# Performance work log

Hardware: AMD Instinct MI355X
Metric: run time of the kernel (lower is better)

Reference implementation:

```python
import jax, jax.numpy as jnp
import numpy as np

S = 128          # spatial grid size per axis
N = 100000       # active voxels
C_IN = 32
C_OUT = 32
FS = 3           # filter size per axis -> 27 offsets


def _build_rulebook():
    """Build submanifold-conv rulebook: for each active site and each of the
    27 filter offsets, the index of the active neighbor (or masked out)."""
    rng = np.random.default_rng(0)
    coords = rng.integers(0, S, size=(2 * N, 3))
    lin = coords[:, 0] * S * S + coords[:, 1] * S + coords[:, 2]
    lin = np.unique(lin)[:N]                      # sorted unique active sites
    xyz = np.stack([lin // (S * S), (lin // S) % S, lin % S], axis=1)  # [N,3]
    offs = np.stack(np.meshgrid(*([np.arange(FS) - FS // 2] * 3), indexing='ij'), -1).reshape(-1, 3)  # [27,3]
    nb = xyz[:, None, :] + offs[None, :, :]       # [N,27,3]
    inb = np.all((nb >= 0) & (nb < S), axis=-1)   # in-bounds
    nb_lin = nb[..., 0] * S * S + nb[..., 1] * S + nb[..., 2]
    pos = np.searchsorted(lin, nb_lin)
    pos_c = np.clip(pos, 0, N - 1)
    found = inb & (lin[pos_c] == nb_lin)
    nbr_idx = np.where(found, pos_c, 0).astype(np.int32)   # [N,27]
    return nbr_idx, found


def setup_inputs() -> dict:
    key = jax.random.key(0)
    k1, k2 = jax.random.split(key)
    nbr_idx, nbr_mask = _build_rulebook()
    K = FS ** 3
    std = (2.0 / C_IN / K) ** 0.5   # matches module init
    return {
        'features': jax.random.normal(k1, (N, C_IN), dtype=jnp.float32),
        'weight': std * jax.random.normal(k2, (K, C_IN, C_OUT), dtype=jnp.float32),
        'bias': jnp.zeros((C_OUT,), dtype=jnp.float32),
        'nbr_idx': jnp.asarray(nbr_idx),
        'nbr_mask': jnp.asarray(nbr_mask),
    }


def reference(features, weight, bias, nbr_idx, nbr_mask):
    # Submanifold sparse conv: gather active neighbors per filter offset,
    # multiply by per-offset [Cin,Cout] weight, accumulate at active sites.
    gathered = jnp.where(nbr_mask[:, :, None], features[nbr_idx], 0.0)  # [N,K,Cin]
    out = jnp.einsum('nki,kio->no', gathered, weight) + bias            # [N,Cout]
    return out
```

## Files before the change

kernel.cpp:

```cpp
#include <hip/hip_runtime.h>
#include <hip/hip_bf16.h>

#define NVOX 100000
#define CIN 32
#define COUT 32
#define KOFF 27
#define NTILE 6250
#define SENTE (NVOX << 6)

typedef __attribute__((ext_vector_type(8))) short short8;
typedef __attribute__((ext_vector_type(4))) float float4v;
typedef __attribute__((ext_vector_type(4))) int   int4v;

__device__ __forceinline__ short f2bf(float x) {
    union { float f; unsigned u; } v; v.f = x;
    unsigned u = v.u;
    u += 0x7FFFu + ((u >> 16) & 1u);
    return (short)(u >> 16);
}

#define FEAT_BLOCKS 3126

__global__ __launch_bounds__(256) void cvt_kernel(
    const float* __restrict__ feat, const float* __restrict__ weight,
    unsigned short* __restrict__ fbf, short8* __restrict__ wfrag)
{
    if (blockIdx.x < FEAT_BLOCKS) {
        int i = (blockIdx.x * 256 + threadIdx.x) * 4;
        if (i < NVOX * CIN) {
            float4v f = *(const float4v*)(feat + i);
            short s[4] = { f2bf(f.x), f2bf(f.y), f2bf(f.z), f2bf(f.w) };
            *(ulonglong1*)(fbf + i) = *(ulonglong1*)s;
        } else if (i < (NVOX + 1) * CIN) {
            short s[4] = { 0, 0, 0, 0 };
            *(ulonglong1*)(fbf + i) = *(ulonglong1*)s;
        }
    } else {
        int g = (blockIdx.x - FEAT_BLOCKS) * 256 + threadIdx.x;
        if (g >= KOFF * 2 * 64) return;
        int k   = g >> 7;
        int rem = g & 127;
        int t   = rem >> 6;
        int ln  = rem & 63;
        int co  = t * 16 + (ln & 15);
        int cib = (ln >> 4) * 8;
        const float* wp = weight + (k * CIN + cib) * COUT + co;
        short8 b;
#pragma unroll
        for (int j = 0; j < 8; ++j) b[j] = f2bf(wp[j * COUT]);
        wfrag[g] = b;
    }
}

__global__ __launch_bounds__(512, 4) void subm_conv_kernel(
    const unsigned short* __restrict__ fbf,
    const short8* __restrict__ wfrag,
    const float* __restrict__ bias,
    const int* __restrict__ nbr_idx,
    const int* __restrict__ nbr_mask,
    float* __restrict__ out)
{
    __shared__ short8 wlds[KOFF * 2 * 64];
    __shared__ int    mstore[8 * 576];

    const int tid  = threadIdx.x;
    const int lane = tid & 63;
    const int wave = tid >> 6;
    const int m    = lane & 15;
    const int quad = lane >> 4;

    const int bid  = blockIdx.x;
    const int xcd  = bid & 7;
    const int bi   = bid >> 3;
    const int bswz = (xcd < 6) ? xcd * 98 + bi : 588 + (xcd - 6) * 97 + bi;

    const int tile0 = bswz * 8 + wave;
    const bool tv   = tile0 < NTILE;
    const int tile  = tv ? tile0 : (NTILE - 1);
    const int v0    = tile * 16;

    short8 wreg[7];
#pragma unroll
    for (int u = 0; u < 7; ++u) {
        int g = tid + u * 512;
        if (g < KOFF * 2 * 64) wreg[u] = wfrag[g];
    }

    int* meta = mstore + wave * 576;
    {
        const int tb = v0 * KOFF;
        const int j0 = lane * 4;
        int4v ia = __builtin_nontemporal_load((const int4v*)(nbr_idx  + tb + j0));
        int4v ma = __builtin_nontemporal_load((const int4v*)(nbr_mask + tb + j0));
#pragma unroll
        for (int c = 0; c < 4; ++c) {
            int j = j0 + c;
            meta[(j / 27) * 28 + (j % 27)] = (ma[c] ? ia[c] : NVOX) << 6;
        }
        if (j0 < 176) {
            int4v ib = __builtin_nontemporal_load((const int4v*)(nbr_idx  + tb + 256 + j0));
            int4v mb = __builtin_nontemporal_load((const int4v*)(nbr_mask + tb + 256 + j0));
#pragma unroll
            for (int c = 0; c < 4; ++c) {
                int j = 256 + j0 + c;
                meta[(j / 27) * 28 + (j % 27)] = (mb[c] ? ib[c] : NVOX) << 6;
            }
        }
    }

    int enc[28];
    {
        const int4v* mp = (const int4v*)(meta + m * 28);
#pragma unroll
        for (int i = 0; i < 7; ++i) {
            int4v t = mp[i];
            enc[i * 4 + 0] = t.x; enc[i * 4 + 1] = t.y;
            enc[i * 4 + 2] = t.z; enc[i * 4 + 3] = t.w;
        }
    }

    unsigned bmv = 0;
#pragma unroll
    for (int k = 0; k < KOFF; ++k)
        bmv |= (__any(enc[k] != SENTE) ? 1u : 0u) << k;
    const unsigned bm = (unsigned)__builtin_amdgcn_readfirstlane((int)bmv);

#pragma unroll
    for (int u = 0; u < 7; ++u) {
        int g = tid + u * 512;
        if (g < KOFF * 2 * 64) wlds[g] = wreg[u];
    }

    const char* fb   = (const char*)fbf;
    const int   boff = quad * 16;

    short8 abuf[8];
#pragma unroll
    for (int k = 0; k < 8; ++k)
        abuf[k] = *(const short8*)(fb + (size_t)(unsigned)enc[k] + boff);

    __syncthreads();

    float4v acc0 = {0.f, 0.f, 0.f, 0.f};
    float4v acc1 = {0.f, 0.f, 0.f, 0.f};

#pragma unroll
    for (int k = 0; k < KOFF; ++k) {
        const int slot = k & 7;
        short8 a = abuf[slot];
        if (k + 8 < KOFF)
            abuf[slot] = *(const short8*)(fb + (size_t)(unsigned)enc[k + 8] + boff);

        if (bm & (1u << k)) {
            short8 wb0 = wlds[k * 128 + lane];
            short8 wb1 = wlds[k * 128 + 64 + lane];
            acc0 = __builtin_amdgcn_mfma_f32_16x16x32_bf16(a, wb0, acc0, 0, 0, 0);
            acc1 = __builtin_amdgcn_mfma_f32_16x16x32_bf16(a, wb1, acc1, 0, 0, 0);
        }
    }

    float* tb = (float*)(mstore + wave * 576);

    const float bs0 = bias[m];
    const float bs1 = bias[16 + m];
    if (tv) {
#pragma unroll
        for (int r = 0; r < 4; ++r) {
            tb[(quad * 4 + r) * 36 + m]      = acc0[r] + bs0;
            tb[(quad * 4 + r) * 36 + 16 + m] = acc1[r] + bs1;
        }
#pragma unroll
        for (int p = 0; p < 2; ++p) {
            int flat = p * 64 + lane;
            int row  = flat >> 3;
            int ch   = flat & 7;
            float4v val = *(const float4v*)(tb + row * 36 + ch * 4);
            __builtin_nontemporal_store(val, (float4v*)(out + (size_t)(v0 + row) * COUT + ch * 4));
        }
    }
}

extern "C" void kernel_launch(void* const* d_in, const int* in_sizes, int n_in,
                              void* d_out, int out_size, void* d_ws, size_t ws_size,
                              hipStream_t stream) {
    const float* feat = (const float*)d_in[0];
    const float* wgt  = (const float*)d_in[1];
    const float* bias = (const float*)d_in[2];
    const int*   nidx = (const int*)d_in[3];
    const int*   nmsk = (const int*)d_in[4];
    float*       out  = (float*)d_out;

    char* ws = (char*)d_ws;
    unsigned short* fbf   = (unsigned short*)ws;
    short8*         wfrag = (short8*)(ws + 6400128);

    const int wgt_blocks = (KOFF * 2 * 64 + 255) / 256;
    cvt_kernel<<<FEAT_BLOCKS + wgt_blocks, 256, 0, stream>>>(feat, wgt, fbf, wfrag);

    const int block = 512;
    const int grid  = (NTILE + 7) / 8;
    subm_conv_kernel<<<grid, block, 0, stream>>>(fbf, wfrag, bias, nidx, nmsk, out);
}
```

Before: 98.49 us.

## Fuse bf16 conversion into conv kernel, gather fp32 features directly

Removes the separate conversion kernel. The conv kernel now gathers fp32 feature rows directly and converts them to bf16 in registers before the MFMA, and each block converts the weights into LDS itself. Masked neighbours are encoded with a low-bit flag and zeroed after conversion, so no padded zero row is needed. This saves one launch and a full pass over the features, but doubles the bytes per gathered row and repeats the weight conversion in every block.

```diff
diff --git a/kernel.cpp b/kernel.cpp
--- a/kernel.cpp
+++ b/kernel.cpp
@@ -6,55 +6,14 @@
 #define COUT 32
 #define KOFF 27
 #define NTILE 6250
-#define SENTE (NVOX << 6)
 
 typedef __attribute__((ext_vector_type(8))) short short8;
 typedef __attribute__((ext_vector_type(4))) float float4v;
 typedef __attribute__((ext_vector_type(4))) int   int4v;
 
-__device__ __forceinline__ short f2bf(float x) {
-    union { float f; unsigned u; } v; v.f = x;
-    unsigned u = v.u;
-    u += 0x7FFFu + ((u >> 16) & 1u);
-    return (short)(u >> 16);
-}
-
-#define FEAT_BLOCKS 3126
-
-__global__ __launch_bounds__(256) void cvt_kernel(
-    const float* __restrict__ feat, const float* __restrict__ weight,
-    unsigned short* __restrict__ fbf, short8* __restrict__ wfrag)
-{
-    if (blockIdx.x < FEAT_BLOCKS) {
-        int i = (blockIdx.x * 256 + threadIdx.x) * 4;
-        if (i < NVOX * CIN) {
-            float4v f = *(const float4v*)(feat + i);
-            short s[4] = { f2bf(f.x), f2bf(f.y), f2bf(f.z), f2bf(f.w) };
-            *(ulonglong1*)(fbf + i) = *(ulonglong1*)s;
-        } else if (i < (NVOX + 1) * CIN) {
-            short s[4] = { 0, 0, 0, 0 };
-            *(ulonglong1*)(fbf + i) = *(ulonglong1*)s;
-        }
-    } else {
-        int g = (blockIdx.x - FEAT_BLOCKS) * 256 + threadIdx.x;
-        if (g >= KOFF * 2 * 64) return;
-        int k   = g >> 7;
-        int rem = g & 127;
-        int t   = rem >> 6;
-        int ln  = rem & 63;
-        int co  = t * 16 + (ln & 15);
-        int cib = (ln >> 4) * 8;
-        const float* wp = weight + (k * CIN + cib) * COUT + co;
-        short8 b;
-#pragma unroll
-        for (int j = 0; j < 8; ++j) b[j] = f2bf(wp[j * COUT]);
-        wfrag[g] = b;
-    }
-}
-
 __global__ __launch_bounds__(512, 4) void subm_conv_kernel(
-    const unsigned short* __restrict__ fbf,
-    const short8* __restrict__ wfrag,
+    const float* __restrict__ feat,
+    const float* __restrict__ weight,
     const float* __restrict__ bias,
     const int* __restrict__ nbr_idx,
     const int* __restrict__ nbr_mask,
@@ -79,13 +38,6 @@
     const int tile  = tv ? tile0 : (NTILE - 1);
     const int v0    = tile * 16;
 
-    short8 wreg[7];
-#pragma unroll
-    for (int u = 0; u < 7; ++u) {
-        int g = tid + u * 512;
-        if (g < KOFF * 2 * 64) wreg[u] = wfrag[g];
-    }
-
     int* meta = mstore + wave * 576;
     {
         const int tb = v0 * KOFF;
@@ -95,7 +47,7 @@
 #pragma unroll
         for (int c = 0; c < 4; ++c) {
             int j = j0 + c;
-            meta[(j / 27) * 28 + (j % 27)] = (ma[c] ? ia[c] : NVOX) << 6;
+            meta[(j / 27) * 28 + (j % 27)] = ma[c] ? (ia[c] << 7) : 1;
         }
         if (j0 < 176) {
             int4v ib = __builtin_nontemporal_load((const int4v*)(nbr_idx  + tb + 256 + j0));
@@ -103,8 +55,29 @@
 #pragma unroll
             for (int c = 0; c < 4; ++c) {
                 int j = 256 + j0 + c;
-                meta[(j / 27) * 28 + (j % 27)] = (mb[c] ? ib[c] : NVOX) << 6;
+                meta[(j / 27) * 28 + (j % 27)] = mb[c] ? (ib[c] << 7) : 1;
             }
+        }
+    }
+
+    {
+        const int co  = (tid & 15) + (((tid >> 6) & 1) << 4) * 0;
+    }
+#pragma unroll
+    for (int u = 0; u < 7; ++u) {
+        int g = tid + u * 512;
+        if (g < KOFF * 2 * 64) {
+            int k   = g >> 7;
+            int rem = g & 127;
+            int t   = rem >> 6;
+            int ln  = rem & 63;
+            int co  = t * 16 + (ln & 15);
+            int cib = (ln >> 4) * 8;
+            const float* wp = weight + (k * CIN + cib) * COUT + co;
+            union { short8 s8; __bf16 b[8]; } cw;
+#pragma unroll
+            for (int j = 0; j < 8; ++j) cw.b[j] = (__bf16)wp[j * COUT];
+            wlds[g] = cw.s8;
         }
     }
 
@@ -122,22 +95,20 @@
     unsigned bmv = 0;
 #pragma unroll
     for (int k = 0; k < KOFF; ++k)
-        bmv |= (__any(enc[k] != SENTE) ? 1u : 0u) << k;
+        bmv |= (__any(!(enc[k] & 1)) ? 1u : 0u) << k;
     const unsigned bm = (unsigned)__builtin_amdgcn_readfirstlane((int)bmv);
 
+    const char* fb   = (const char*)feat;
+    const int   boff = quad * 32;
+
+    float4v a0[6], a1[6];
 #pragma unroll
-    for (int u = 0; u < 7; ++u) {
-        int g = tid + u * 512;
-        if (g < KOFF * 2 * 64) wlds[g] = wreg[u];
+    for (int k = 0; k < 6; ++k) {
+        unsigned e = (unsigned)enc[k];
+        const char* p = fb + (e & ~127u) + boff;
+        a0[k] = *(const float4v*)p;
+        a1[k] = *(const float4v*)(p + 16);
     }
-
-    const char* fb   = (const char*)fbf;
-    const int   boff = quad * 16;
-
-    short8 abuf[8];
-#pragma unroll
-    for (int k = 0; k < 8; ++k)
-        abuf[k] = *(const short8*)(fb + (size_t)(unsigned)enc[k] + boff);
 
     __syncthreads();
 
@@ -146,12 +117,27 @@
 
 #pragma unroll
     for (int k = 0; k < KOFF; ++k) {
-        const int slot = k & 7;
-        short8 a = abuf[slot];
-        if (k + 8 < KOFF)
-            abuf[slot] = *(const short8*)(fb + (size_t)(unsigned)enc[k + 8] + boff);
+        const int slot = k % 6;
+        float4v f0 = a0[slot];
+        float4v f1 = a1[slot];
+        const unsigned ecur = (unsigned)enc[k];
+        if (k + 6 < KOFF) {
+            unsigned en = (unsigned)enc[k + 6];
+            const char* pn = fb + (en & ~127u) + boff;
+            a0[slot] = *(const float4v*)pn;
+            a1[slot] = *(const float4v*)(pn + 16);
+        }
 
         if (bm & (1u << k)) {
+            union { short8 s8; unsigned u4[4]; __bf16 b[8]; } cu;
+            cu.b[0] = (__bf16)f0.x; cu.b[1] = (__bf16)f0.y;
+            cu.b[2] = (__bf16)f0.z; cu.b[3] = (__bf16)f0.w;
+            cu.b[4] = (__bf16)f1.x; cu.b[5] = (__bf16)f1.y;
+            cu.b[6] = (__bf16)f1.z; cu.b[7] = (__bf16)f1.w;
+            if (ecur & 1u) {
+                cu.u4[0] = 0; cu.u4[1] = 0; cu.u4[2] = 0; cu.u4[3] = 0;
+            }
+            short8 a = cu.s8;
             short8 wb0 = wlds[k * 128 + lane];
             short8 wb1 = wlds[k * 128 + 64 + lane];
             acc0 = __builtin_amdgcn_mfma_f32_16x16x32_bf16(a, wb0, acc0, 0, 0, 0);
@@ -190,14 +176,7 @@
     const int*   nmsk = (const int*)d_in[4];
     float*       out  = (float*)d_out;
 
-    char* ws = (char*)d_ws;
-    unsigned short* fbf   = (unsigned short*)ws;
-    short8*         wfrag = (short8*)(ws + 6400128);
-
-    const int wgt_blocks = (KOFF * 2 * 64 + 255) / 256;
-    cvt_kernel<<<FEAT_BLOCKS + wgt_blocks, 256, 0, stream>>>(feat, wgt, fbf, wfrag);
-
     const int block = 512;
     const int grid  = (NTILE + 7) / 8;
-    subm_conv_kernel<<<grid, block, 0, stream>>>(fbf, wfrag, bias, nidx, nmsk, out);
+    subm_conv_kernel<<<grid, block, 0, stream>>>(feat, wgt, bias, nidx, nmsk, out);
 }
```

Result: slower. 108.6 us (+10.2%).
